# Optimization experiments

Hardware: AMD Instinct MI355X
Metric: run time of the kernel (lower is better)

The kernel has to match this reference:

```python
import jax, jax.numpy as jnp
import numpy as np

B, S, D, H, N = 8, 1024, 1024, 16, 16  # batch, seq, hidden, heads, num_ns_tokens
HD = D // H


def setup_inputs() -> dict:
    key = jax.random.key(0)
    ks = jax.random.split(key, 8)
    s = 0.02
    return {
        "x": jax.random.normal(ks[0], (B, S, D), jnp.float32),
        "Wq_shared": jax.random.normal(ks[1], (D, D), jnp.float32) * s,
        "Wk_shared": jax.random.normal(ks[2], (D, D), jnp.float32) * s,
        "Wv_shared": jax.random.normal(ks[3], (D, D), jnp.float32) * s,
        "Wq_ded": jax.random.normal(ks[4], (N, D, D), jnp.float32) * s,
        "Wk_ded": jax.random.normal(ks[5], (N, D, D), jnp.float32) * s,
        "Wv_ded": jax.random.normal(ks[6], (N, D, D), jnp.float32) * s,
        "Wo": jax.random.normal(ks[7], (D, D), jnp.float32) * s,
    }


def reference(x, Wq_shared, Wk_shared, Wv_shared, Wq_ded, Wk_ded, Wv_ded, Wo):
    b, s, d = x.shape
    n = Wq_ded.shape[0]

    def proj(Ws, Wd):
        shared = x @ Ws                                   # [b,s,d]
        ded = jnp.einsum('bnd,ndo->bno', x[:, :n], Wd)    # first n tokens use dedicated weights
        return jnp.concatenate([ded, shared[:, n:]], axis=1)

    q = proj(Wq_shared, Wq_ded).reshape(b, s, H, HD)
    k = proj(Wk_shared, Wk_ded).reshape(b, s, H, HD)
    v = proj(Wv_shared, Wv_ded).reshape(b, s, H, HD)

    scores = jnp.einsum('bqhd,bkhd->bhqk', q, k) / jnp.sqrt(jnp.float32(HD))
    causal = jnp.tril(jnp.ones((s, s), dtype=bool))
    scores = jnp.where(causal, scores, jnp.float32(-1e9))
    attn = jax.nn.softmax(scores, axis=-1)
    out = jnp.einsum('bhqk,bkhd->bqhd', attn, v).reshape(b, s, d)
    output = out @ Wo
    return (output, k, v)
```

## Files before the change

kernel.cpp:

```cpp
#include <hip/hip_runtime.h>
#include <cstdint>


typedef unsigned short u16;
typedef __attribute__((ext_vector_type(8)))  __bf16 bf16x8;
typedef __attribute__((ext_vector_type(8)))  u16    u16x8;
typedef __attribute__((ext_vector_type(4)))  float  f32x4;

#define BSD   (8u * 1024u * 1024u)
#define QSCALE 0.18033688011112042f

__device__ __forceinline__ u16 f2bf(float f) {
    unsigned u = __builtin_bit_cast(unsigned, f);
    u += 0x7fffu + ((u >> 16) & 1u);
    return (u16)(u >> 16);
}

__device__ __forceinline__ unsigned pack_bf2(float p0, float p1) {
    return __builtin_amdgcn_perm(__builtin_bit_cast(unsigned, p1),
                                 __builtin_bit_cast(unsigned, p0), 0x07060302u);
}

__device__ __forceinline__ void gl_lds16(const void* g, void* l) {
    __builtin_amdgcn_global_load_lds(
        (const __attribute__((address_space(1))) unsigned*)g,
        (__attribute__((address_space(3))) unsigned*)l, 16, 0, 0);
}

#define FENCE asm volatile("" ::: "memory")
#define WAITV(n) asm volatile("s_waitcnt vmcnt(" #n ")" ::: "memory")

__global__ __launch_bounds__(256) void cvt_fused(
        const float* __restrict__ Wq, const float* __restrict__ Wk,
        const float* __restrict__ Wv, const float* __restrict__ Wo,
        u16* __restrict__ WTcat, u16* __restrict__ WoT,
        const float4* __restrict__ x, u16* __restrict__ xb) {
    __shared__ float t[32][33];
    int z = blockIdx.z;
    if (z < 4) {
        const float* src = (z == 0) ? Wq : (z == 1) ? Wk : (z == 2) ? Wv : Wo;
        u16* dst = (z < 3) ? (WTcat + (size_t)z * 1024 * 1024) : WoT;
        int k0 = blockIdx.x * 32, n0 = blockIdx.y * 32;
        int xx = threadIdx.x & 31, yy = threadIdx.x >> 5;
#pragma unroll
        for (int i = 0; i < 4; ++i)
            t[yy + 8 * i][xx] = src[(size_t)(k0 + yy + 8 * i) * 1024 + n0 + xx];
        __syncthreads();
#pragma unroll
        for (int i = 0; i < 4; ++i)
            dst[(size_t)(n0 + yy + 8 * i) * 1024 + k0 + xx] = f2bf(t[xx][yy + 8 * i]);
    } else {
        int lb = (z - 4) * 1024 + blockIdx.y * 32 + blockIdx.x;
        int i = lb * 256 + threadIdx.x;
        float4 v = x[i];
        ushort4 o;
        o.x = f2bf(v.x); o.y = f2bf(v.y); o.z = f2bf(v.z); o.w = f2bf(v.w);
        ((ushort4*)xb)[i] = o;
    }
}

#define LDfrag(BUF, bufi, row, ks)                                            \
    __builtin_bit_cast(bf16x8, *(const u16x8*)&BUF[bufi]                      \
        [(row) * 64 + ((((ks) * 4 + kg) ^ ((row) & 7)) * 8)])

#define PH(bufi, mh, nh, STAGE_STMT, GATE_STMT) do {                          \
    bf16x8 af_[2][2], bq_[2][2];                                              \
    _Pragma("unroll") for (int mi = 0; mi < 2; ++mi) {                        \
        int arow = wm * 64 + (mh) * 32 + mi * 16 + lr;                        \
        _Pragma("unroll") for (int ks = 0; ks < 2; ++ks)                      \
            af_[mi][ks] = LDfrag(As, bufi, arow, ks);                         \
    }                                                                         \
    _Pragma("unroll") for (int ni = 0; ni < 2; ++ni) {                        \
        int brow = wn * 64 + (nh) * 32 + ni * 16 + lr;                        \
        _Pragma("unroll") for (int ks = 0; ks < 2; ++ks)                      \
            bq_[ni][ks] = LDfrag(Bs, bufi, brow, ks);                         \
    }                                                                         \
    STAGE_STMT;                                                               \
    GATE_STMT;                                                                \
    FENCE; __builtin_amdgcn_s_barrier(); FENCE;                               \
    asm volatile("s_waitcnt lgkmcnt(0)" ::: "memory");                        \
    __builtin_amdgcn_s_setprio(1);                                            \
    _Pragma("unroll") for (int ks = 0; ks < 2; ++ks)                          \
    _Pragma("unroll") for (int mi = 0; mi < 2; ++mi)                          \
    _Pragma("unroll") for (int ni = 0; ni < 2; ++ni)                          \
        acc[(mh) * 2 + mi][(nh) * 2 + ni] =                                   \
            __builtin_amdgcn_mfma_f32_16x16x32_bf16(                          \
                af_[mi][ks], bq_[ni][ks],                                     \
                acc[(mh) * 2 + mi][(nh) * 2 + ni], 0, 0, 0);                  \
    __builtin_amdgcn_s_setprio(0);                                            \
    FENCE; __builtin_amdgcn_s_barrier(); FENCE;                               \
} while (0)

template <int MODE>
__global__ __launch_bounds__(512, 2) void gemm8p(
        const u16* __restrict__ A, const u16* __restrict__ Bt,
        float* __restrict__ fout, u16* __restrict__ q_attn,
        u16* __restrict__ k_attn) {
    const int K = 1024, nt = 16;
    __shared__ u16 As[2][128 * 64];
    __shared__ u16 Bs[2][256 * 64];
    int tid = threadIdx.x;
    int w = tid >> 6, lane = tid & 63;
    int m0 = blockIdx.y * 128, n0 = blockIdx.x * 256;
    int wm = w & 1, wn = w >> 1;
    int lr = lane & 15, kg = lane >> 4;

    f32x4 acc[4][4] = {};

    auto stageA = [&](int buf, int half, int t) {
        int ci = ((w & 3) << 6) + lane + ((w >> 2) << 9) + (half << 8);
        int row = ci >> 3, cg = (ci & 7) ^ (row & 7);
        gl_lds16(A + (size_t)(m0 + row) * K + t * 64 + cg * 8, &As[buf][ci * 8]);
    };
    auto stageB = [&](int buf, int half, int t) {
#pragma unroll
        for (int j = 0; j < 2; ++j) {
            int u = w + 8 * j;
            int ci = ((u >> 2) << 9) + ((u & 3) << 6) + lane + (half << 8);
            int row = ci >> 3, cg = (ci & 7) ^ (row & 7);
            gl_lds16(Bt + (size_t)(n0 + row) * K + t * 64 + cg * 8, &Bs[buf][ci * 8]);
        }
    };

    stageA(0, 0, 0);
    stageB(0, 0, 0);
    stageA(0, 1, 0);
    stageB(0, 1, 0);
    WAITV(3);
    FENCE; __builtin_amdgcn_s_barrier(); FENCE;

    for (int t = 0; t < nt - 1; ++t) {
        int cur = t & 1, nxt = cur ^ 1;
        PH(cur, 0, 0, stageA(nxt, 0, t + 1), WAITV(3));
        PH(cur, 1, 0, stageB(nxt, 0, t + 1), WAITV(3));
        PH(cur, 1, 1, stageA(nxt, 1, t + 1), ((void)0));
        PH(cur, 0, 1, stageB(nxt, 1, t + 1), WAITV(3));
    }
    PH(1, 0, 0, ((void)0), WAITV(2));
    PH(1, 1, 0, ((void)0), WAITV(0));
    PH(1, 1, 1, ((void)0), ((void)0));
    PH(1, 0, 1, ((void)0), ((void)0));

    if (MODE == 1) {
#pragma unroll
        for (int am = 0; am < 4; ++am) {
            int mbase = m0 + wm * 64 + am * 16 + kg * 4;
#pragma unroll
            for (int bn = 0; bn < 4; ++bn) {
                int col = n0 + wn * 64 + bn * 16 + lr;
#pragma unroll
                for (int r = 0; r < 4; ++r)
                    fout[(size_t)(mbase + r) * 1024 + col] = acc[am][bn][r];
            }
        }
    } else {
        int matId = n0 >> 10;
        int ncol0 = (n0 & 1023) + wn * 64;
#pragma unroll
        for (int am = 0; am < 4; ++am) {
            int mbase = m0 + wm * 64 + am * 16 + kg * 4;
#pragma unroll
            for (int bn = 0; bn < 4; ++bn) {
                int col = ncol0 + bn * 16 + lr;
#pragma unroll
                for (int r = 0; r < 4; ++r) {
                    int mm = mbase + r;
                    float v = acc[am][bn][r];
                    size_t idx = (size_t)mm * 1024 + col;
                    if (matId == 0) {
                        q_attn[idx] = f2bf(v * QSCALE);
                    } else if (matId == 1) {
                        fout[(size_t)BSD + idx] = v;
                        k_attn[idx] = f2bf(v);
                    } else {
                        fout[(size_t)2 * BSD + idx] = v;
                    }
                }
            }
        }
    }
}

__global__ __launch_bounds__(256) void ded_partial(
        const float* __restrict__ x, const float* __restrict__ Wq,
        const float* __restrict__ Wk, const float* __restrict__ Wv,
        float* __restrict__ part) {
    int dc = blockIdx.x, n = blockIdx.y, mat = blockIdx.z;
    const float* W = ((mat == 0) ? Wq : (mat == 1) ? Wk : Wv) +
                     (size_t)n * 1024 * 1024;
    __shared__ float xs[8 * 128];
    int t = threadIdx.x;
    for (int i = t; i < 1024; i += 256) {
        int b = i >> 7, d = i & 127;
        xs[i] = x[((size_t)b * 1024 + n) * 1024 + dc * 128 + d];
    }
    __syncthreads();
    int o0 = t * 4;
    float4 acc[8];
#pragma unroll
    for (int b = 0; b < 8; ++b) acc[b] = make_float4(0.f, 0.f, 0.f, 0.f);
    for (int d = 0; d < 128; d += 4) {
        float4 w0 = *(const float4*)&W[(size_t)(dc * 128 + d + 0) * 1024 + o0];
        float4 w1 = *(const float4*)&W[(size_t)(dc * 128 + d + 1) * 1024 + o0];
        float4 w2 = *(const float4*)&W[(size_t)(dc * 128 + d + 2) * 1024 + o0];
        float4 w3 = *(const float4*)&W[(size_t)(dc * 128 + d + 3) * 1024 + o0];
#pragma unroll
        for (int b = 0; b < 8; ++b) {
            float x0 = xs[b * 128 + d], x1 = xs[b * 128 + d + 1];
            float x2 = xs[b * 128 + d + 2], x3 = xs[b * 128 + d + 3];
            acc[b].x += x0 * w0.x + x1 * w1.x + x2 * w2.x + x3 * w3.x;
            acc[b].y += x0 * w0.y + x1 * w1.y + x2 * w2.y + x3 * w3.y;
            acc[b].z += x0 * w0.z + x1 * w1.z + x2 * w2.z + x3 * w3.z;
            acc[b].w += x0 * w0.w + x1 * w1.w + x2 * w2.w + x3 * w3.w;
        }
    }
#pragma unroll
    for (int b = 0; b < 8; ++b)
        *(float4*)&part[(size_t)(((mat * 8 + dc) * 8 + b) * 16 + n) * 1024 + o0] = acc[b];
}

__global__ __launch_bounds__(256) void fix_vt(
        const float* __restrict__ part, float* __restrict__ d_out,
        u16* __restrict__ q_attn, u16* __restrict__ k_attn,
        const float* __restrict__ vf, u16* __restrict__ vT) {
    __shared__ float t[64][65];
    int bid = blockIdx.x;
    int tid = threadIdx.x;

    if (bid < 384) {
        int mat = bid >> 7, b = (bid >> 4) & 7, n = bid & 15;
        int o0 = tid * 4;
        float v[4] = {0.f, 0.f, 0.f, 0.f};
        for (int dc = 0; dc < 8; ++dc) {
            float4 p = *(const float4*)&part[(size_t)(((mat * 8 + dc) * 8 + b) * 16 + n) * 1024 + o0];
            v[0] += p.x; v[1] += p.y; v[2] += p.z; v[3] += p.w;
        }
#pragma unroll
        for (int j = 0; j < 4; ++j) {
            int col = o0 + j;
            size_t idx = ((size_t)b * 1024 + n) * 1024 + col;
            if (mat == 0) {
                q_attn[idx] = f2bf(v[j] * QSCALE);
            } else if (mat == 1) {
                d_out[(size_t)BSD + idx] = v[j];
                k_attn[idx] = f2bf(v[j]);
            } else {
                d_out[(size_t)2 * BSD + idx] = v[j];
                int h = col >> 6, hd = col & 63;
                vT[((size_t)((b * 16 + h) * 64 + hd)) * 1024 + n] = f2bf(v[j]);
            }
        }
        return;
    }

    int id = bid - 384;
    int st = id & 15, h = (id >> 4) & 15, b = id >> 8;
    int cg = tid & 15, sl = tid >> 4;
#pragma unroll
    for (int p = 0; p < 4; ++p) {
        int s = p * 16 + sl;
        float4 v = *(const float4*)&vf[
            ((size_t)(b * 1024 + st * 64 + s)) * 1024 + h * 64 + cg * 4];
        t[cg * 4 + 0][s] = v.x;
        t[cg * 4 + 1][s] = v.y;
        t[cg * 4 + 2][s] = v.z;
        t[cg * 4 + 3][s] = v.w;
    }
    __syncthreads();
    int hd = tid >> 2, sc = (tid & 3) * 16;
    if (st == 0 && sc == 0) return;
    u16* dst = vT + ((size_t)((b * 16 + h) * 64 + hd)) * 1024 + st * 64 + sc;
#pragma unroll
    for (int c = 0; c < 4; ++c) {
        ushort4 o;
        o.x = f2bf(t[hd][sc + c * 4 + 0]);
        o.y = f2bf(t[hd][sc + c * 4 + 1]);
        o.z = f2bf(t[hd][sc + c * 4 + 2]);
        o.w = f2bf(t[hd][sc + c * 4 + 3]);
        *(ushort4*)(dst + c * 4) = o;
    }
}

__global__ __launch_bounds__(256) void attn(
        const u16* __restrict__ q_attn, const u16* __restrict__ k_attn,
        const u16* __restrict__ vT, u16* __restrict__ O) {
    int qt = 7 - blockIdx.x;
    int h = blockIdx.y, b = blockIdx.z;
    const u16* Qg = q_attn + ((size_t)(b * 1024) + qt * 128) * 1024 + h * 64;
    const u16* Kg = k_attn + ((size_t)(b * 1024)) * 1024 + h * 64;
    const u16* Vg = vT + (size_t)((b * 16 + h) * 64) * 1024;

    __shared__ u16 Qs[128 * 64];
    __shared__ u16 Ks[64 * 64];
    __shared__ u16 Vs[64 * 64];
    __shared__ u16 Ps[128 * 64];
    __shared__ float red[4 * 32];

    int tid = threadIdx.x, wave = tid >> 6, lane = tid & 63;
    int lr = lane & 15, kg = lane >> 4;

#pragma unroll
    for (int j = 0; j < 4; ++j) {
        int ci = j * 256 + tid;
        int row = ci >> 3, cg = (ci & 7) ^ (row & 7);
        gl_lds16(Qg + (size_t)row * 1024 + cg * 8, Qs + ci * 8);
    }

    float l_acc[2] = {0.f, 0.f};
    f32x4 oacc[2][4] = {};

    int nkt = 2 * qt + 2;
    for (int kt = 0; kt < nkt; ++kt) {
        __syncthreads();
#pragma unroll
        for (int j = 0; j < 2; ++j) {
            int ci = j * 256 + tid;
            int row = ci >> 3, cg = (ci & 7) ^ (row & 7);
            gl_lds16(Kg + (size_t)(kt * 64 + row) * 1024 + cg * 8, Ks + ci * 8);
            gl_lds16(Vg + (size_t)row * 1024 + kt * 64 + cg * 8, Vs + ci * 8);
        }
        __syncthreads();

        bool wactive = (qt * 128 + wave * 32 + 31) >= kt * 64;
        if (wactive) {
            f32x4 sacc[4][2] = {};
#pragma unroll
            for (int ks = 0; ks < 2; ++ks) {
                bf16x8 af[4], bq[2];
#pragma unroll
                for (int mi = 0; mi < 4; ++mi) {
                    int row = mi * 16 + lr;
                    af[mi] = __builtin_bit_cast(bf16x8,
                        *(const u16x8*)&Ks[row * 64 + (((ks * 4 + kg) ^ (row & 7)) * 8)]);
                }
#pragma unroll
                for (int nj = 0; nj < 2; ++nj) {
                    int qr = wave * 32 + nj * 16 + lr;
                    bq[nj] = __builtin_bit_cast(bf16x8,
                        *(const u16x8*)&Qs[qr * 64 + (((ks * 4 + kg) ^ (qr & 7)) * 8)]);
                }
#pragma unroll
                for (int mi = 0; mi < 4; ++mi)
#pragma unroll
                    for (int nj = 0; nj < 2; ++nj)
                        sacc[mi][nj] = __builtin_amdgcn_mfma_f32_16x16x32_bf16(
                            af[mi], bq[nj], sacc[mi][nj], 0, 0, 0);
            }

            if (kt >= 2 * qt) {
#pragma unroll
                for (int mi = 0; mi < 4; ++mi)
#pragma unroll
                    for (int nj = 0; nj < 2; ++nj)
#pragma unroll
                        for (int r = 0; r < 4; ++r) {
                            int kk_g = kt * 64 + mi * 16 + kg * 4 + r;
                            int q_g  = qt * 128 + wave * 32 + nj * 16 + lr;
                            if (kk_g > q_g) sacc[mi][nj][r] = -1e30f;
                        }
            }

#pragma unroll
            for (int nj = 0; nj < 2; ++nj) {
                int q = wave * 32 + nj * 16 + lr;
                float lsum = 0.f;
#pragma unroll
                for (int mi = 0; mi < 4; ++mi) {
                    float p0 = __builtin_amdgcn_exp2f(sacc[mi][nj][0]);
                    float p1 = __builtin_amdgcn_exp2f(sacc[mi][nj][1]);
                    float p2 = __builtin_amdgcn_exp2f(sacc[mi][nj][2]);
                    float p3 = __builtin_amdgcn_exp2f(sacc[mi][nj][3]);
                    lsum += (p0 + p1) + (p2 + p3);
                    int kkc = mi * 2 + (kg >> 1);
                    int off = q * 64 + ((kkc ^ (q & 7)) * 8) + (kg & 1) * 4;
                    uint2 w2;
                    w2.x = pack_bf2(p0, p1);
                    w2.y = pack_bf2(p2, p3);
                    *(uint2*)&Ps[off] = w2;
                }
                l_acc[nj] += lsum;
            }

#pragma unroll
            for (int ks = 0; ks < 2; ++ks) {
                bf16x8 ap[2], bv[4];
#pragma unroll
                for (int mi = 0; mi < 2; ++mi) {
                    int q = wave * 32 + mi * 16 + lr;
                    ap[mi] = __builtin_bit_cast(bf16x8,
                        *(const u16x8*)&Ps[q * 64 + (((ks * 4 + kg) ^ (q & 7)) * 8)]);
                }
#pragma unroll
                for (int nj = 0; nj < 4; ++nj) {
                    int hd = nj * 16 + lr;
                    bv[nj] = __builtin_bit_cast(bf16x8,
                        *(const u16x8*)&Vs[hd * 64 + (((ks * 4 + kg) ^ (hd & 7)) * 8)]);
                }
#pragma unroll
                for (int mi = 0; mi < 2; ++mi)
#pragma unroll
                    for (int nj = 0; nj < 4; ++nj)
                        oacc[mi][nj] = __builtin_amdgcn_mfma_f32_16x16x32_bf16(
                            ap[mi], bv[nj], oacc[mi][nj], 0, 0, 0);
            }
        }
    }

#pragma unroll
    for (int nj = 0; nj < 2; ++nj) {
        float l = l_acc[nj];
        l += __shfl_xor(l, 16);
        l += __shfl_xor(l, 32);
        if (kg == 0) red[wave * 32 + nj * 16 + lr] = l;
    }
#pragma unroll
    for (int mi = 0; mi < 2; ++mi) {
        f32x4 lv = *(f32x4*)&red[wave * 32 + mi * 16 + kg * 4];
        f32x4 rv;
#pragma unroll
        for (int r = 0; r < 4; ++r) rv[r] = __builtin_amdgcn_rcpf(lv[r]);
#pragma unroll
        for (int nj = 0; nj < 4; ++nj)
#pragma unroll
            for (int r = 0; r < 4; ++r) {
                int q_local = wave * 32 + mi * 16 + kg * 4 + r;
                size_t row = (size_t)b * 1024 + qt * 128 + q_local;
                O[row * 1024 + h * 64 + nj * 16 + lr] =
                    f2bf(oacc[mi][nj][r] * rv[r]);
            }
    }
}

extern "C" void kernel_launch(void* const* d_in, const int* in_sizes, int n_in,
                              void* d_out, int out_size, void* d_ws, size_t ws_size,
                              hipStream_t stream) {
    const float* x   = (const float*)d_in[0];
    const float* Wq  = (const float*)d_in[1];
    const float* Wk  = (const float*)d_in[2];
    const float* Wv  = (const float*)d_in[3];
    const float* Wqd = (const float*)d_in[4];
    const float* Wkd = (const float*)d_in[5];
    const float* Wvd = (const float*)d_in[6];
    const float* Wo  = (const float*)d_in[7];
    float* out = (float*)d_out;

    char* ws = (char*)d_ws;
    u16*   WTcat  = (u16*)(ws);
    u16*   WoT    = (u16*)(ws + 6291456);
    u16*   xb     = (u16*)(ws + 8388608);
    u16*   q_attn = (u16*)(ws + 25165824);
    u16*   k_attn = (u16*)(ws + 41943040);
    u16*   vT     = (u16*)(ws + 58720256);
    u16*   Ow     = (u16*)(ws + 75497472);
    float* part   = (float*)(ws + 92274688);

    cvt_fused<<<dim3(32, 32, 12), 256, 0, stream>>>(
        Wq, Wk, Wv, Wo, WTcat, WoT, (const float4*)x, xb);
    gemm8p<0><<<dim3(12, 64), 512, 0, stream>>>(xb, WTcat, out, q_attn, k_attn);
    ded_partial<<<dim3(8, 16, 3), 256, 0, stream>>>(x, Wqd, Wkd, Wvd, part);
    fix_vt<<<dim3(2432), 256, 0, stream>>>(
        part, out, q_attn, k_attn, out + (size_t)2 * BSD, vT);
    attn<<<dim3(8, 16, 8), 256, 0, stream>>>(q_attn, k_attn, vT, Ow);
    gemm8p<1><<<dim3(4, 64), 512, 0, stream>>>(Ow, WoT, out, nullptr, nullptr);
}
```

Before: 474.3 us.

## Replace QKV GEMM 8-phase ping-pong schedule with simpler double-buffered loop

```diff
diff --git a/kernel.cpp b/kernel.cpp
--- a/kernel.cpp
+++ b/kernel.cpp
@@ -56,6 +56,121 @@
         ushort4 o;
         o.x = f2bf(v.x); o.y = f2bf(v.y); o.z = f2bf(v.z); o.w = f2bf(v.w);
         ((ushort4*)xb)[i] = o;
+    }
+}
+
+__global__ __launch_bounds__(512, 2) void gemm_qkv(
+        const u16* __restrict__ A, const u16* __restrict__ Bt,
+        float* __restrict__ fout, u16* __restrict__ q_attn,
+        u16* __restrict__ k_attn) {
+    const int K = 1024, NT = 16;
+    __shared__ u16 As[2][128 * 64];
+    __shared__ u16 Bs[2][256 * 64];
+    int tid = threadIdx.x;
+    int w = tid >> 6, lane = tid & 63;
+    int m0 = blockIdx.y * 128, n0 = blockIdx.x * 256;
+    int wm = w & 1, wn = w >> 1;
+    int lr = lane & 15, kg = lane >> 4;
+
+    f32x4 acc[4][4] = {};
+
+    auto stageAll = [&](int buf, int t) {
+#pragma unroll
+        for (int s = 0; s < 2; ++s) {
+            int ci = s * 512 + tid;
+            int row = ci >> 3, cg = (ci & 7) ^ (row & 7);
+            gl_lds16(A + (size_t)(m0 + row) * K + t * 64 + cg * 8, &As[buf][ci * 8]);
+        }
+#pragma unroll
+        for (int s = 0; s < 4; ++s) {
+            int ci = s * 512 + tid;
+            int row = ci >> 3, cg = (ci & 7) ^ (row & 7);
+            gl_lds16(Bt + (size_t)(n0 + row) * K + t * 64 + cg * 8, &Bs[buf][ci * 8]);
+        }
+    };
+
+    stageAll(0, 0);
+    WAITV(0);
+    FENCE; __builtin_amdgcn_s_barrier(); FENCE;
+
+    for (int t = 0; t < NT; ++t) {
+        int cur = t & 1, nxt = cur ^ 1;
+        {
+            bf16x8 af[4], bf[4];
+#pragma unroll
+            for (int mi = 0; mi < 4; ++mi) {
+                int row = wm * 64 + mi * 16 + lr;
+                af[mi] = __builtin_bit_cast(bf16x8,
+                    *(const u16x8*)&As[cur][row * 64 + ((kg ^ (row & 7)) * 8)]);
+            }
+#pragma unroll
+            for (int ni = 0; ni < 4; ++ni) {
+                int row = wn * 64 + ni * 16 + lr;
+                bf[ni] = __builtin_bit_cast(bf16x8,
+                    *(const u16x8*)&Bs[cur][row * 64 + ((kg ^ (row & 7)) * 8)]);
+            }
+            if (t < NT - 1) stageAll(nxt, t + 1);
+            __builtin_amdgcn_s_setprio(1);
+#pragma unroll
+            for (int mi = 0; mi < 4; ++mi)
+#pragma unroll
+                for (int ni = 0; ni < 4; ++ni)
+                    acc[mi][ni] = __builtin_amdgcn_mfma_f32_16x16x32_bf16(
+                        af[mi], bf[ni], acc[mi][ni], 0, 0, 0);
+            __builtin_amdgcn_s_setprio(0);
+        }
+        {
+            bf16x8 af[4], bf[4];
+#pragma unroll
+            for (int mi = 0; mi < 4; ++mi) {
+                int row = wm * 64 + mi * 16 + lr;
+                af[mi] = __builtin_bit_cast(bf16x8,
+                    *(const u16x8*)&As[cur][row * 64 + (((4 + kg) ^ (row & 7)) * 8)]);
+            }
+#pragma unroll
+            for (int ni = 0; ni < 4; ++ni) {
+                int row = wn * 64 + ni * 16 + lr;
+                bf[ni] = __builtin_bit_cast(bf16x8,
+                    *(const u16x8*)&Bs[cur][row * 64 + (((4 + kg) ^ (row & 7)) * 8)]);
+            }
+            __builtin_amdgcn_s_setprio(1);
+#pragma unroll
+            for (int mi = 0; mi < 4; ++mi)
+#pragma unroll
+                for (int ni = 0; ni < 4; ++ni)
+                    acc[mi][ni] = __builtin_amdgcn_mfma_f32_16x16x32_bf16(
+                        af[mi], bf[ni], acc[mi][ni], 0, 0, 0);
+            __builtin_amdgcn_s_setprio(0);
+        }
+        if (t < NT - 1) {
+            WAITV(0);
+            FENCE; __builtin_amdgcn_s_barrier(); FENCE;
+        }
+    }
+
+    int matId = n0 >> 10;
+    int ncol0 = (n0 & 1023) + wn * 64;
+#pragma unroll
+    for (int am = 0; am < 4; ++am) {
+        int mbase = m0 + wm * 64 + am * 16 + kg * 4;
+#pragma unroll
+        for (int bn = 0; bn < 4; ++bn) {
+            int col = ncol0 + bn * 16 + lr;
+#pragma unroll
+            for (int r = 0; r < 4; ++r) {
+                int mm = mbase + r;
+                float v = acc[am][bn][r];
+                size_t idx = (size_t)mm * 1024 + col;
+                if (matId == 0) {
+                    q_attn[idx] = f2bf(v * QSCALE);
+                } else if (matId == 1) {
+                    fout[(size_t)BSD + idx] = v;
+                    k_attn[idx] = f2bf(v);
+                } else {
+                    fout[(size_t)2 * BSD + idx] = v;
+                }
+            }
+        }
     }
 }
 
@@ -91,11 +206,9 @@
     FENCE; __builtin_amdgcn_s_barrier(); FENCE;                               \
 } while (0)
 
-template <int MODE>
-__global__ __launch_bounds__(512, 2) void gemm8p(
+__global__ __launch_bounds__(512, 2) void gemm8p_wo(
         const u16* __restrict__ A, const u16* __restrict__ Bt,
-        float* __restrict__ fout, u16* __restrict__ q_attn,
-        u16* __restrict__ k_attn) {
+        float* __restrict__ fout) {
     const int K = 1024, nt = 16;
     __shared__ u16 As[2][128 * 64];
     __shared__ u16 Bs[2][256 * 64];
@@ -141,42 +254,15 @@
     PH(1, 1, 1, ((void)0), ((void)0));
     PH(1, 0, 1, ((void)0), ((void)0));
 
-    if (MODE == 1) {
-#pragma unroll
-        for (int am = 0; am < 4; ++am) {
-            int mbase = m0 + wm * 64 + am * 16 + kg * 4;
-#pragma unroll
-            for (int bn = 0; bn < 4; ++bn) {
-                int col = n0 + wn * 64 + bn * 16 + lr;
-#pragma unroll
-                for (int r = 0; r < 4; ++r)
-                    fout[(size_t)(mbase + r) * 1024 + col] = acc[am][bn][r];
-            }
-        }
-    } else {
-        int matId = n0 >> 10;
-        int ncol0 = (n0 & 1023) + wn * 64;
-#pragma unroll
-        for (int am = 0; am < 4; ++am) {
-            int mbase = m0 + wm * 64 + am * 16 + kg * 4;
-#pragma unroll
-            for (int bn = 0; bn < 4; ++bn) {
-                int col = ncol0 + bn * 16 + lr;
-#pragma unroll
-                for (int r = 0; r < 4; ++r) {
-                    int mm = mbase + r;
-                    float v = acc[am][bn][r];
-                    size_t idx = (size_t)mm * 1024 + col;
-                    if (matId == 0) {
-                        q_attn[idx] = f2bf(v * QSCALE);
-                    } else if (matId == 1) {
-                        fout[(size_t)BSD + idx] = v;
-                        k_attn[idx] = f2bf(v);
-                    } else {
-                        fout[(size_t)2 * BSD + idx] = v;
-                    }
-                }
-            }
+#pragma unroll
+    for (int am = 0; am < 4; ++am) {
+        int mbase = m0 + wm * 64 + am * 16 + kg * 4;
+#pragma unroll
+        for (int bn = 0; bn < 4; ++bn) {
+            int col = n0 + wn * 64 + bn * 16 + lr;
+#pragma unroll
+            for (int r = 0; r < 4; ++r)
+                fout[(size_t)(mbase + r) * 1024 + col] = acc[am][bn][r];
         }
     }
 }
@@ -456,10 +542,10 @@
 
     cvt_fused<<<dim3(32, 32, 12), 256, 0, stream>>>(
         Wq, Wk, Wv, Wo, WTcat, WoT, (const float4*)x, xb);
-    gemm8p<0><<<dim3(12, 64), 512, 0, stream>>>(xb, WTcat, out, q_attn, k_attn);
+    gemm_qkv<<<dim3(12, 64), 512, 0, stream>>>(xb, WTcat, out, q_attn, k_attn);
     ded_partial<<<dim3(8, 16, 3), 256, 0, stream>>>(x, Wqd, Wkd, Wvd, part);
     fix_vt<<<dim3(2432), 256, 0, stream>>>(
         part, out, q_attn, k_attn, out + (size_t)2 * BSD, vT);
     attn<<<dim3(8, 16, 8), 256, 0, stream>>>(q_attn, k_attn, vT, Ow);
-    gemm8p<1><<<dim3(4, 64), 512, 0, stream>>>(Ow, WoT, out, nullptr, nullptr);
-}
+    gemm8p_wo<<<dim3(4, 64), 512, 0, stream>>>(Ow, WoT, out);
+}
```

Result: faster. 459.0 us (-3.2%).
